# Kernel tuning notes

Hardware: AMD Instinct MI355X
Metric: run time of the kernel (lower is better)

The kernel has to match this reference:

```python
import jax, jax.numpy as jnp
import numpy as np
from jax import lax

BETA = 1e-07
LAMBDA_TV = 1e-08


def _resize_bilinear_ac(x, out_h, out_w):
    """Bilinear resize with align_corners=True, NCHW layout (matches F.interpolate)."""
    B, C, H, W = x.shape
    ys = jnp.arange(out_h, dtype=jnp.float32) * ((H - 1) / max(out_h - 1, 1))
    xs = jnp.arange(out_w, dtype=jnp.float32) * ((W - 1) / max(out_w - 1, 1))
    y0 = jnp.floor(ys).astype(jnp.int32); y1 = jnp.minimum(y0 + 1, H - 1)
    x0 = jnp.floor(xs).astype(jnp.int32); x1 = jnp.minimum(x0 + 1, W - 1)
    wy = (ys - y0.astype(jnp.float32))[:, None]   # [out_h,1]
    wx = (xs - x0.astype(jnp.float32))[None, :]   # [1,out_w]
    r0 = x[:, :, y0, :]; r1 = x[:, :, y1, :]      # [B,C,out_h,W]
    top = r0[:, :, :, x0] * (1.0 - wx) + r0[:, :, :, x1] * wx
    bot = r1[:, :, :, x0] * (1.0 - wx) + r1[:, :, :, x1] * wx
    return top * (1.0 - wy) + bot * wy


def _levelset_loss(output, target):
    B = output.shape[0]
    # pcentroid computed under no_grad in torch -> stop_gradient here
    num = jnp.einsum('bthw,bchw->btc', target, output)
    den = jnp.sum(output, axis=(2, 3))                       # [B,C]
    pcent = lax.stop_gradient(num / den[:, None, :])          # [B,T,C]
    plevel = target[:, :, None, :, :] - pcent[:, :, :, None, None]  # [B,T,C,H,W]
    return jnp.sum(plevel * plevel * output[:, None]) / B


def _gradient_loss2d(output):
    B = output.shape[0]
    dH = jnp.abs(output[:, :, 1:, :] - output[:, :, :-1, :])
    dW = jnp.abs(output[:, :, :, 1:] - output[:, :, :, :-1])
    return (jnp.sum(dH) + jnp.sum(dW)) / B


def _nonlocal_tv_loss(f_output, f_sem):
    B, Cs, H, W = f_sem.shape
    N = H * W
    fo = _resize_bilinear_ac(f_output, H, W)                  # [B,C,H,W]
    C = fo.shape[1]
    # F.normalize(f_sem, dim=1) (eps=1e-12)
    norm = jnp.sqrt(jnp.sum(f_sem * f_sem, axis=1, keepdims=True))
    sem = f_sem / jnp.maximum(norm, 1e-12)
    sem_f = sem.reshape(B, Cs, N)
    # tau[b,r,p] = relu(<sem_r, sem_p>); normalized by global spatial max per (b,r)
    tau = jax.nn.relu(jnp.einsum('bcr,bcp->brp', sem_f, sem_f))  # [B,N,N]
    tau_max = jnp.max(tau, axis=2, keepdims=True)
    tau_n = tau / (tau_max + 1e-05)
    # torch.matmul(dL[B,C,H,W], tau[B,1,H,W]) summed over everything reduces to
    # sum_{i,k,j} dL[b,c,i,k] * tau[b,k,j] = sum_k (sum_i dL[b,c,i,k]) * (sum_j tau[b,k,j])
    t = tau_n.reshape(B, N, H, W).sum(axis=3)                 # [B,N,H] row-sums of tau
    of = fo.reshape(B, C, N)
    # dL[b,c,r,h,w] = |out_r - out_{(h,w)}| (penalty='l1')
    dL = jnp.abs(of[:, :, :, None, None] - fo[:, :, None, :, :])  # [B,C,N,H,W]
    A = dL.sum(axis=3)                                         # [B,C,N,W] sum over rows i
    return jnp.einsum('bcrk,brk->', A, t) / B


def setup_inputs() -> dict:
    key = jax.random.key(0)
    k1, k2, k3, k4 = jax.random.split(key, 4)
    return {
        'output': jax.random.uniform(k1, (4, 21, 512, 512), dtype=jnp.float32),
        'target': jax.random.uniform(k2, (4, 3, 512, 512), dtype=jnp.float32),
        'f_sem': jax.random.normal(k3, (4, 256, 32, 32), dtype=jnp.float32),
        'f_output': jax.random.uniform(k4, (4, 21, 64, 64), dtype=jnp.float32),
        'use_NonLocal_TV': 1,
    }


def reference(output, target, f_sem, f_output, use_NonLocal_TV):
    loss_LS = _levelset_loss(output, target)
    if use_NonLocal_TV:
        loss_TV = _nonlocal_tv_loss(f_output, f_sem) * LAMBDA_TV
    else:
        loss_TV = _gradient_loss2d(output) * LAMBDA_TV
    loss_MS = (loss_LS + loss_TV) * BETA
    return (loss_LS * BETA, loss_TV * BETA, loss_MS)
```

## Files before the change

### kernel.cpp

```cpp
#include <hip/hip_runtime.h>

#define BETA_F   1e-7f
#define LAMBDA_F 1e-8f

#define HWSZ 262144
#define NBC  84
#define NPIX 1024

#define OFF_FO    0
#define OFF_GSUM  86016
#define OFF_INVN  (86016 + 131072)
#define OFF_RMAX  (217088 + 4096)
#define OFF_LS    (221184 + 4096)
#define OFF_ACC   (225280 + 588)
#define ZERO_START OFF_RMAX
#define ZERO_COUNT (4096 + 588 + 4)

__global__ __launch_bounds__(256) void k_prep(const float* __restrict__ fo_in,
                                              const float* __restrict__ fsem,
                                              float* __restrict__ ws) {
    const int bid = blockIdx.x, tid = threadIdx.x;
    if (bid < 19) {
        int i = bid * 256 + tid;
        if (i < ZERO_COUNT) ws[ZERO_START + i] = 0.f;
    } else if (bid < 103) {
        const int bc = bid - 19;
        const float* im = fo_in + bc * 4096;
        for (int p = tid; p < 1024; p += 256) {
            const int oy = p >> 5, ox = p & 31;
            const float R = 63.0f / 31.0f;
            float sy = oy * R, sx = ox * R;
            int y0 = (int)sy, x0 = (int)sx;
            int y1 = min(y0 + 1, 63), x1 = min(x0 + 1, 63);
            float wy = sy - (float)y0, wx = sx - (float)x0;
            float v00 = im[y0 * 64 + x0], v01 = im[y0 * 64 + x1];
            float v10 = im[y1 * 64 + x0], v11 = im[y1 * 64 + x1];
            float top = v00 * (1.f - wx) + v01 * wx;
            float bot = v10 * (1.f - wx) + v11 * wx;
            ws[OFF_FO + bc * NPIX + p] = top * (1.f - wy) + bot * wy;
        }
    } else {
        const int blk = bid - 103;
        const int b = blk >> 4, pg = blk & 15;
        const int p0 = pg * 64;
        const int pi = tid & 63, cg = tid >> 6;
        float s = 0.f;
        for (int c = cg; c < 256; c += 4) {
            float v = fsem[(b * 256 + c) * 1024 + p0 + pi];
            s += v * v;
        }
        __shared__ float red[4][64];
        red[cg][pi] = s;
        __syncthreads();
        if (tid < 64) {
            float t = red[0][tid] + red[1][tid] + red[2][tid] + red[3][tid];
            ws[OFF_INVN + b * 1024 + p0 + tid] = 1.f / fmaxf(sqrtf(t), 1e-12f);
        }
    }
}

__device__ __forceinline__ int swz(int p4, int k) {
    int s = (p4 >> 1) | ((p4 & 1) << 4);
    return s ^ (k & 7);
}

__global__ __launch_bounds__(256) void k_main(const float* __restrict__ outp,
                                              const float* __restrict__ tgt,
                                              const float* __restrict__ fsem,
                                              float* __restrict__ ws) {
    __shared__ __align__(16) char smem[68096];
    const int tid = threadIdx.x;

    if (blockIdx.x < 256) {
        float4* As4    = (float4*)smem;
        float4* Bs4    = (float4*)(smem + 32768);
        float*  gsum_s = (float*)(smem + 65536);
        int*    rmax_s = (int*)(smem + 67584);
        const int bid = blockIdx.x;
        const int ct = bid & 7, rt = (bid >> 3) & 7, b = bid >> 6;
        const int r0 = rt * 128, c0 = ct * 128;
        for (int i = tid; i < 512; i += 256) gsum_s[i] = 0.f;
        if (tid < 128) rmax_s[tid] = 0;

        const int tr = tid >> 4, tc = tid & 15;
        float acc[8][8];
        #pragma unroll
        for (int i = 0; i < 8; ++i)
            #pragma unroll
            for (int j = 0; j < 8; ++j) acc[i][j] = 0.f;

        const int kl = tid >> 5, p4s = tid & 31;
        for (int kk = 0; kk < 4; ++kk) {
            __syncthreads();
            #pragma unroll
            for (int q = 0; q < 8; ++q) {
                int k = kl + q * 8;
                const float* srcA = &fsem[(b * 256 + kk * 64 + k) * 1024 + r0 + p4s * 4];
                const float* srcB = &fsem[(b * 256 + kk * 64 + k) * 1024 + c0 + p4s * 4];
                float4 va = *(const float4*)srcA;
                float4 vb = *(const float4*)srcB;
                int sl = swz(p4s, k);
                As4[k * 32 + sl] = va;
                Bs4[k * 32 + sl] = vb;
            }
            __syncthreads();
            #pragma unroll 4
            for (int k = 0; k < 64; ++k) {
                int k7 = k & 7;
                float4 a0 = As4[k * 32 + (tr ^ k7)];
                float4 a1 = As4[k * 32 + ((tr ^ k7) | 16)];
                float4 b0 = Bs4[k * 32 + (tc ^ k7)];
                float4 b1 = Bs4[k * 32 + ((tc ^ k7) | 16)];
                float a[8]  = {a0.x, a0.y, a0.z, a0.w, a1.x, a1.y, a1.z, a1.w};
                float bb[8] = {b0.x, b0.y, b0.z, b0.w, b1.x, b1.y, b1.z, b1.w};
                #pragma unroll
                for (int i = 0; i < 8; ++i)
                    #pragma unroll
                    for (int j = 0; j < 8; ++j)
                        acc[i][j] += a[i] * bb[j];
            }
        }

        float ir[8], ic[8];
        #pragma unroll
        for (int i = 0; i < 8; ++i) {
            ir[i] = ws[OFF_INVN + b * 1024 + r0 + tr * 8 + i];
            ic[i] = ws[OFF_INVN + b * 1024 + c0 + tc * 8 + i];
        }
        const int g = tc >> 2;
        #pragma unroll
        for (int i = 0; i < 8; ++i) {
            float s = 0.f, m = 0.f;
            #pragma unroll
            for (int j = 0; j < 8; ++j) {
                float v = fmaxf(acc[i][j], 0.f) * ir[i] * ic[j];
                s += v;
                m = fmaxf(m, v);
            }
            int row = tr * 8 + i;
            atomicAdd(&gsum_s[row * 4 + g], s);
            atomicMax(&rmax_s[row], __float_as_int(m));
        }
        __syncthreads();
        for (int i = tid; i < 512; i += 256) {
            int row = i >> 2, gg = i & 3;
            ws[OFF_GSUM + (b * 1024 + r0 + row) * 32 + ct * 4 + gg] = gsum_s[i];
        }
        if (tid < 128)
            atomicMax((int*)&ws[OFF_RMAX + b * 1024 + r0 + tid], rmax_s[tid]);
    } else {
        float (*red)[7] = (float (*)[7])smem;
        const int blk = blockIdx.x - 256;
        const int slice = blk & 31, bc = blk >> 5;
        const int b = bc / 21;
        const float4* o4 = (const float4*)(outp + (size_t)bc * HWSZ + slice * 8192);
        const float4* t4 = (const float4*)(tgt + (size_t)b * (3 * HWSZ) + slice * 8192);
        float n0 = 0, n1 = 0, n2 = 0, q0 = 0, q1 = 0, q2 = 0, dn = 0;
        #pragma unroll 2
        for (int i = tid; i < 2048; i += 256) {
            float4 o  = o4[i];
            float4 ta = t4[i];
            float4 tb = t4[i + 65536];
            float4 tc = t4[i + 131072];
            dn += o.x + o.y + o.z + o.w;
            n0 += ta.x*o.x + ta.y*o.y + ta.z*o.z + ta.w*o.w;
            q0 += ta.x*ta.x*o.x + ta.y*ta.y*o.y + ta.z*ta.z*o.z + ta.w*ta.w*o.w;
            n1 += tb.x*o.x + tb.y*o.y + tb.z*o.z + tb.w*o.w;
            q1 += tb.x*tb.x*o.x + tb.y*tb.y*o.y + tb.z*tb.z*o.z + tb.w*tb.w*o.w;
            n2 += tc.x*o.x + tc.y*o.y + tc.z*o.z + tc.w*o.w;
            q2 += tc.x*tc.x*o.x + tc.y*tc.y*o.y + tc.z*tc.z*o.z + tc.w*tc.w*o.w;
        }
        float vals[7] = {n0, n1, n2, q0, q1, q2, dn};
        #pragma unroll
        for (int j = 0; j < 7; ++j) {
            float v = vals[j];
            #pragma unroll
            for (int off = 32; off; off >>= 1) v += __shfl_xor(v, off);
            if ((tid & 63) == 0) red[tid >> 6][j] = v;
        }
        __syncthreads();
        if (tid < 7) {
            float s = red[0][tid] + red[1][tid] + red[2][tid] + red[3][tid];
            atomicAdd(&ws[OFF_LS + bc * 7 + tid], s);
        }
    }
}

__global__ __launch_bounds__(256) void k_tv(const float* __restrict__ ws,
                                            float* __restrict__ acc_out) {
    const int bc = blockIdx.y;
    const int b = bc / 21;
    const int tid = threadIdx.x;
    __shared__ float4 fo4[256];
    const float4* src = (const float4*)(ws + OFF_FO + bc * NPIX);
    fo4[tid] = src[tid];
    __syncthreads();
    const int r = blockIdx.x * 256 + tid;
    const float v = ((const float*)fo4)[r];
    float ak[32];
    #pragma unroll
    for (int k = 0; k < 32; ++k) ak[k] = 0.f;
    #pragma unroll 4
    for (int h = 0; h < 32; ++h) {
        #pragma unroll
        for (int k4 = 0; k4 < 8; ++k4) {
            float4 f = fo4[h * 8 + k4];
            ak[k4 * 4 + 0] += fabsf(v - f.x);
            ak[k4 * 4 + 1] += fabsf(v - f.y);
            ak[k4 * 4 + 2] += fabsf(v - f.z);
            ak[k4 * 4 + 3] += fabsf(v - f.w);
        }
    }
    const float rm = ws[OFF_RMAX + b * 1024 + r];
    const float inv = 1.f / (rm + 1e-5f);
    const float* t = ws + OFF_GSUM + (b * 1024 + r) * 32;
    float dot = 0.f;
    #pragma unroll
    for (int k = 0; k < 32; ++k) dot += ak[k] * t[k];
    float part = dot * inv;
    #pragma unroll
    for (int off = 32; off; off >>= 1) part += __shfl_xor(part, off);
    __shared__ float red[4];
    if ((tid & 63) == 0) red[tid >> 6] = part;
    __syncthreads();
    if (tid == 0) atomicAdd(acc_out, red[0] + red[1] + red[2] + red[3]);
}

__global__ void k_combine(const float* __restrict__ ws, float* __restrict__ out) {
    const int tid = threadIdx.x;
    float v = 0.f;
    if (tid < NBC) {
        const float* p = ws + OFF_LS + tid * 7;
        float den = p[6];
        v = (p[3] + p[4] + p[5]) - (p[0]*p[0] + p[1]*p[1] + p[2]*p[2]) / den;
    }
    #pragma unroll
    for (int off = 32; off; off >>= 1) v += __shfl_xor(v, off);
    __shared__ float red[2];
    if ((tid & 63) == 0) red[tid >> 6] = v;
    __syncthreads();
    if (tid == 0) {
        float lsv = (red[0] + red[1]) * 0.25f;
        float tvv = ws[OFF_ACC] * 0.25f;
        out[0] = lsv * BETA_F;
        out[1] = tvv * LAMBDA_F * BETA_F;
        out[2] = (lsv + tvv * LAMBDA_F) * BETA_F;
    }
}

extern "C" void kernel_launch(void* const* d_in, const int* in_sizes, int n_in,
                              void* d_out, int out_size, void* d_ws, size_t ws_size,
                              hipStream_t stream) {
    const float* output   = (const float*)d_in[0];
    const float* target   = (const float*)d_in[1];
    const float* f_sem    = (const float*)d_in[2];
    const float* f_output = (const float*)d_in[3];
    float* ws  = (float*)d_ws;
    float* out = (float*)d_out;

    hipLaunchKernelGGL(k_prep,    dim3(167),    dim3(256), 0, stream, f_output, f_sem, ws);
    hipLaunchKernelGGL(k_main,    dim3(2944),   dim3(256), 0, stream, output, target, f_sem, ws);
    hipLaunchKernelGGL(k_tv,      dim3(4, 84),  dim3(256), 0, stream, ws, ws + OFF_ACC);
    hipLaunchKernelGGL(k_combine, dim3(1),      dim3(128), 0, stream, ws, out);
}
```

Before: 224.5 us.

## Exploit Gram matrix symmetry: compute only upper-triangular tiles, shrink K-chunk to 16

The sem Gram matrix is symmetric, so only the 36 upper-triangular 128x128 tiles per batch are computed instead of 64. Each off-diagonal block also emits column-wise partial sums and maxima for the mirrored tile. The K staging chunk drops from 64 to 16, which cuts shared memory from about 68KB to 21KB and should raise occupancy for both the gram and the streaming level-set blocks. The trade-off is more syncthreads per tile and a second epilogue pass on off-diagonal tiles.

```diff
diff --git a/kernel.cpp b/kernel.cpp
--- a/kernel.cpp
+++ b/kernel.cpp
@@ -15,6 +15,13 @@
 #define OFF_ACC   (225280 + 588)
 #define ZERO_START OFF_RMAX
 #define ZERO_COUNT (4096 + 588 + 4)
+
+#define N_GRAM_BLK 144
+
+__device__ const unsigned char RT_[36] =
+    {0,0,0,0,0,0,0,0, 1,1,1,1,1,1,1, 2,2,2,2,2,2, 3,3,3,3,3, 4,4,4,4, 5,5,5, 6,6, 7};
+__device__ const unsigned char CT_[36] =
+    {0,1,2,3,4,5,6,7, 1,2,3,4,5,6,7, 2,3,4,5,6,7, 3,4,5,6,7, 4,5,6,7, 5,6,7, 6,7, 7};
 
 __global__ __launch_bounds__(256) void k_prep(const float* __restrict__ fo_in,
                                               const float* __restrict__ fsem,
@@ -68,19 +75,23 @@
                                               const float* __restrict__ tgt,
                                               const float* __restrict__ fsem,
                                               float* __restrict__ ws) {
-    __shared__ __align__(16) char smem[68096];
+    __shared__ __align__(16) char smem[21504];
     const int tid = threadIdx.x;
 
-    if (blockIdx.x < 256) {
+    if (blockIdx.x < N_GRAM_BLK) {
         float4* As4    = (float4*)smem;
-        float4* Bs4    = (float4*)(smem + 32768);
-        float*  gsum_s = (float*)(smem + 65536);
-        int*    rmax_s = (int*)(smem + 67584);
+        float4* Bs4    = (float4*)(smem + 8192);
+        float*  gs_row = (float*)(smem + 16384);
+        float*  gs_col = (float*)(smem + 18432);
+        int*    rm_row = (int*)(smem + 20480);
+        int*    rm_col = (int*)(smem + 20992);
         const int bid = blockIdx.x;
-        const int ct = bid & 7, rt = (bid >> 3) & 7, b = bid >> 6;
+        const int b = bid / 36, t = bid % 36;
+        const int rt = RT_[t], ct = CT_[t];
+        const bool diag = (rt == ct);
         const int r0 = rt * 128, c0 = ct * 128;
-        for (int i = tid; i < 512; i += 256) gsum_s[i] = 0.f;
-        if (tid < 128) rmax_s[tid] = 0;
+        for (int i = tid; i < 512; i += 256) { gs_row[i] = 0.f; gs_col[i] = 0.f; }
+        if (tid < 128) { rm_row[tid] = 0; rm_col[tid] = 0; }
 
         const int tr = tid >> 4, tc = tid & 15;
         float acc[8][8];
@@ -90,13 +101,13 @@
             for (int j = 0; j < 8; ++j) acc[i][j] = 0.f;
 
         const int kl = tid >> 5, p4s = tid & 31;
-        for (int kk = 0; kk < 4; ++kk) {
+        for (int kk = 0; kk < 16; ++kk) {
             __syncthreads();
             #pragma unroll
-            for (int q = 0; q < 8; ++q) {
+            for (int q = 0; q < 2; ++q) {
                 int k = kl + q * 8;
-                const float* srcA = &fsem[(b * 256 + kk * 64 + k) * 1024 + r0 + p4s * 4];
-                const float* srcB = &fsem[(b * 256 + kk * 64 + k) * 1024 + c0 + p4s * 4];
+                const float* srcA = &fsem[(b * 256 + kk * 16 + k) * 1024 + r0 + p4s * 4];
+                const float* srcB = &fsem[(b * 256 + kk * 16 + k) * 1024 + c0 + p4s * 4];
                 float4 va = *(const float4*)srcA;
                 float4 vb = *(const float4*)srcB;
                 int sl = swz(p4s, k);
@@ -105,7 +116,7 @@
             }
             __syncthreads();
             #pragma unroll 4
-            for (int k = 0; k < 64; ++k) {
+            for (int k = 0; k < 16; ++k) {
                 int k7 = k & 7;
                 float4 a0 = As4[k * 32 + (tr ^ k7)];
                 float4 a1 = As4[k * 32 + ((tr ^ k7) | 16)];
@@ -127,7 +138,7 @@
             ir[i] = ws[OFF_INVN + b * 1024 + r0 + tr * 8 + i];
             ic[i] = ws[OFF_INVN + b * 1024 + c0 + tc * 8 + i];
         }
-        const int g = tc >> 2;
+        const int gr = tc >> 2;
         #pragma unroll
         for (int i = 0; i < 8; ++i) {
             float s = 0.f, m = 0.f;
@@ -138,19 +149,40 @@
                 m = fmaxf(m, v);
             }
             int row = tr * 8 + i;
-            atomicAdd(&gsum_s[row * 4 + g], s);
-            atomicMax(&rmax_s[row], __float_as_int(m));
+            atomicAdd(&gs_row[row * 4 + gr], s);
+            atomicMax(&rm_row[row], __float_as_int(m));
+        }
+        if (!diag) {
+            const int gc = tr >> 2;
+            #pragma unroll
+            for (int j = 0; j < 8; ++j) {
+                float s = 0.f, m = 0.f;
+                #pragma unroll
+                for (int i = 0; i < 8; ++i) {
+                    float v = fmaxf(acc[i][j], 0.f) * ir[i] * ic[j];
+                    s += v;
+                    m = fmaxf(m, v);
+                }
+                int col = tc * 8 + j;
+                atomicAdd(&gs_col[col * 4 + gc], s);
+                atomicMax(&rm_col[col], __float_as_int(m));
+            }
         }
         __syncthreads();
         for (int i = tid; i < 512; i += 256) {
             int row = i >> 2, gg = i & 3;
-            ws[OFF_GSUM + (b * 1024 + r0 + row) * 32 + ct * 4 + gg] = gsum_s[i];
-        }
-        if (tid < 128)
-            atomicMax((int*)&ws[OFF_RMAX + b * 1024 + r0 + tid], rmax_s[tid]);
+            ws[OFF_GSUM + (b * 1024 + r0 + row) * 32 + ct * 4 + gg] = gs_row[i];
+            if (!diag)
+                ws[OFF_GSUM + (b * 1024 + c0 + row) * 32 + rt * 4 + gg] = gs_col[i];
+        }
+        if (tid < 128) {
+            atomicMax((int*)&ws[OFF_RMAX + b * 1024 + r0 + tid], rm_row[tid]);
+            if (!diag)
+                atomicMax((int*)&ws[OFF_RMAX + b * 1024 + c0 + tid], rm_col[tid]);
+        }
     } else {
         float (*red)[7] = (float (*)[7])smem;
-        const int blk = blockIdx.x - 256;
+        const int blk = blockIdx.x - N_GRAM_BLK;
         const int slice = blk & 31, bc = blk >> 5;
         const int b = bc / 21;
         const float4* o4 = (const float4*)(outp + (size_t)bc * HWSZ + slice * 8192);
@@ -258,8 +290,8 @@
     float* ws  = (float*)d_ws;
     float* out = (float*)d_out;
 
-    hipLaunchKernelGGL(k_prep,    dim3(167),    dim3(256), 0, stream, f_output, f_sem, ws);
-    hipLaunchKernelGGL(k_main,    dim3(2944),   dim3(256), 0, stream, output, target, f_sem, ws);
-    hipLaunchKernelGGL(k_tv,      dim3(4, 84),  dim3(256), 0, stream, ws, ws + OFF_ACC);
-    hipLaunchKernelGGL(k_combine, dim3(1),      dim3(128), 0, stream, ws, out);
-}
+    hipLaunchKernelGGL(k_prep,    dim3(167),            dim3(256), 0, stream, f_output, f_sem, ws);
+    hipLaunchKernelGGL(k_main,    dim3(N_GRAM_BLK+2688),dim3(256), 0, stream, output, target, f_sem, ws);
+    hipLaunchKernelGGL(k_tv,      dim3(4, 84),          dim3(256), 0, stream, ws, ws + OFF_ACC);
+    hipLaunchKernelGGL(k_combine, dim3(1),              dim3(128), 0, stream, ws, out);
+}
```

Result: faster. 216.4 us (-3.6%).
